# Kernel tuning notes

Measured on AMD Instinct MI355X. Metric: run time of the kernel, lower is better.

## Reference

```python
import jax, jax.numpy as jnp
import numpy as np

INPUT_DIM = 1024
CODEBOOK_DIM = 128
CODEBOOK_SIZE = 8192
B, N = 8, 4096


def setup_inputs() -> dict:
    key = jax.random.key(0)
    k1, k2, k3 = jax.random.split(key, 3)
    x = jax.random.normal(k1, (B, N, INPUT_DIM), dtype=jnp.float32)
    # xavier_normal_: std = sqrt(2 / (fan_in + fan_out))
    xavier_std = float(np.sqrt(2.0 / (INPUT_DIM + CODEBOOK_DIM)))
    random_projection = jax.random.normal(k2, (INPUT_DIM, CODEBOOK_DIM), dtype=jnp.float32) * xavier_std
    codebook = jax.random.normal(k3, (CODEBOOK_SIZE, CODEBOOK_DIM), dtype=jnp.float32)
    return {"x": x, "random_projection": random_projection, "codebook": codebook}


def reference(x, random_projection, codebook):
    # random projection: [B, N, D] @ [D, E] -> [B, N, E]
    proj = jnp.einsum("bnd,de->bne", x, random_projection)
    b, n, e = proj.shape
    flat = proj.reshape(b * n, e)  # [BN, E]
    eps = 1e-12  # matches torch F.normalize default eps
    nx = flat / jnp.maximum(jnp.linalg.norm(flat, axis=1, keepdims=True), eps)
    ncb = codebook / jnp.maximum(jnp.linalg.norm(codebook, axis=1, keepdims=True), eps)
    # squared euclidean distances [K, BN]; argmin of d^2 == argmin of cdist
    d2 = (
        jnp.sum(ncb * ncb, axis=1)[:, None]
        + jnp.sum(nx * nx, axis=1)[None, :]
        - 2.0 * (ncb @ nx.T)
    )
    nearest = jnp.argmin(d2, axis=0)  # [BN]
    return nearest.reshape(b, n).astype(jnp.int32)
```

## Files before the change

kernel.cpp:

```cpp
#include <hip/hip_runtime.h>
#include <math.h>
#include <float.h>
#include <limits.h>

#define BN      32768
#define D_IN    1024
#define E_DIM   128
#define CB_N    8192

typedef _Float16 f16x8 __attribute__((ext_vector_type(8)));
typedef _Float16 f16x4 __attribute__((ext_vector_type(4)));
typedef float    f32x4 __attribute__((ext_vector_type(4)));


__global__ __launch_bounds__(256) void pack_cb_kernel(
    const float* __restrict__ cb, _Float16* __restrict__ ph,
    _Float16* __restrict__ pl) {
    __shared__ float L[16][129];
    const int t = threadIdx.x;
    const int g = blockIdx.x;

    const int c = t >> 4, p = t & 15;
    const float4 v0 = *(const float4*)&cb[(size_t)(g * 16 + c) * E_DIM + p * 8];
    const float4 v1 = *(const float4*)&cb[(size_t)(g * 16 + c) * E_DIM + p * 8 + 4];
    float ss = v0.x * v0.x + v0.y * v0.y + v0.z * v0.z + v0.w * v0.w
             + v1.x * v1.x + v1.y * v1.y + v1.z * v1.z + v1.w * v1.w;
#pragma unroll
    for (int m = 1; m < 16; m <<= 1) ss += __shfl_xor(ss, m);
    const float inv = 256.0f / fmaxf(sqrtf(ss), 1e-12f);

    L[c][p * 8 + 0] = v0.x * inv; L[c][p * 8 + 1] = v0.y * inv;
    L[c][p * 8 + 2] = v0.z * inv; L[c][p * 8 + 3] = v0.w * inv;
    L[c][p * 8 + 4] = v1.x * inv; L[c][p * 8 + 5] = v1.y * inv;
    L[c][p * 8 + 6] = v1.z * inv; L[c][p * 8 + 7] = v1.w * inv;
    __syncthreads();

    const int kb = t >> 6, lane = t & 63;
    const int quad = (lane >> 4), col = lane & 15;
    f16x8 h, l;
#pragma unroll
    for (int j = 0; j < 8; ++j) {
        const float v = L[col][kb * 32 + quad * 8 + j];
        const _Float16 hv = (_Float16)v;
        h[j] = hv;
        l[j] = (_Float16)(v - (float)hv);
    }
    const size_t off = ((size_t)(g * 4 + kb) * 64 + lane) * 8;
    *(f16x8*)&ph[off] = h;
    *(f16x8*)&pl[off] = l;
}

__global__ __launch_bounds__(64) void pack_rp_kernel(
    const float* __restrict__ rp, _Float16* __restrict__ rph,
    _Float16* __restrict__ rpl) {
    const int b = blockIdx.x;
    const int kb = b >> 3, nt = b & 7;
    const int lane = threadIdx.x;
    const int quad = lane >> 4, col = lane & 15;
    f16x8 h, l;
#pragma unroll
    for (int j = 0; j < 8; ++j) {
        const float v = rp[(size_t)(kb * 32 + quad * 8 + j) * E_DIM + nt * 16 + col] * 64.0f;
        const _Float16 hv = (_Float16)v;
        h[j] = hv;
        l[j] = (_Float16)(v - (float)hv);
    }
    const size_t off = ((size_t)b * 64 + lane) * 8;
    *(f16x8*)&rph[off] = h;
    *(f16x8*)&rpl[off] = l;
}

#define PAD_ROW 40
#define PPITCH  132

__global__ __launch_bounds__(256, 2) void fused_kernel(
    const float* __restrict__ x,
    const _Float16* __restrict__ rph, const _Float16* __restrict__ rpl,
    const _Float16* __restrict__ ph, const _Float16* __restrict__ pl,
    int* __restrict__ out) {
    __shared__ _Float16 Ah[64 * PAD_ROW];
    __shared__ _Float16 Al[64 * PAD_ROW];
    __shared__ float    P[64 * PPITCH];
    __shared__ float    ls[4][32];
    __shared__ int      li[4][32];

    const int tid  = threadIdx.x;
    const int lane = tid & 63;
    const int w    = tid >> 6;
    const int quad = lane >> 4, col = lane & 15;
    const int qb   = blockIdx.x * 64;

    const int srow = tid >> 3;
    const int skc  = (tid & 7) * 4;

    f32x4 acc[4][2];
#pragma unroll
    for (int mt = 0; mt < 4; ++mt)
#pragma unroll
        for (int h = 0; h < 2; ++h) acc[mt][h] = (f32x4){0.f, 0.f, 0.f, 0.f};

    float4 pre[2];
#pragma unroll
    for (int i = 0; i < 2; ++i)
        pre[i] = *(const float4*)&x[(size_t)(qb + srow + 32 * i) * D_IN + skc];

    for (int kb = 0; kb < 32; ++kb) {
#pragma unroll
        for (int i = 0; i < 2; ++i) {
            const float vv[4] = {pre[i].x, pre[i].y, pre[i].z, pre[i].w};
            f16x4 h4, l4;
#pragma unroll
            for (int j = 0; j < 4; ++j) {
                const float v = vv[j] * 512.0f;
                const _Float16 hv = (_Float16)v;
                h4[j] = hv;
                l4[j] = (_Float16)(v - (float)hv);
            }
            const int base = (srow + 32 * i) * PAD_ROW + skc;
            *(f16x4*)&Ah[base] = h4;
            *(f16x4*)&Al[base] = l4;
        }
        __syncthreads();

        if (kb + 1 < 32) {
#pragma unroll
            for (int i = 0; i < 2; ++i)
                pre[i] = *(const float4*)&x[(size_t)(qb + srow + 32 * i) * D_IN + (kb + 1) * 32 + skc];
        }

        f16x8 bh1[2], bl1[2];
#pragma unroll
        for (int h = 0; h < 2; ++h) {
            const int nt = w * 2 + h;
            const size_t off = ((size_t)(kb * 8 + nt) * 64 + lane) * 8;
            bh1[h] = *(const f16x8*)&rph[off];
            bl1[h] = *(const f16x8*)&rpl[off];
        }

        f16x8 ah1[4], al1[4];
#pragma unroll
        for (int mt = 0; mt < 4; ++mt) {
            const int base = (mt * 16 + col) * PAD_ROW + quad * 8;
            ah1[mt] = *(const f16x8*)&Ah[base];
            al1[mt] = *(const f16x8*)&Al[base];
        }

#pragma unroll
        for (int mt = 0; mt < 4; ++mt)
#pragma unroll
            for (int h = 0; h < 2; ++h)
                acc[mt][h] = __builtin_amdgcn_mfma_f32_16x16x32_f16(ah1[mt], bh1[h], acc[mt][h], 0, 0, 0);
#pragma unroll
        for (int mt = 0; mt < 4; ++mt)
#pragma unroll
            for (int h = 0; h < 2; ++h)
                acc[mt][h] = __builtin_amdgcn_mfma_f32_16x16x32_f16(ah1[mt], bl1[h], acc[mt][h], 0, 0, 0);
#pragma unroll
        for (int mt = 0; mt < 4; ++mt)
#pragma unroll
            for (int h = 0; h < 2; ++h)
                acc[mt][h] = __builtin_amdgcn_mfma_f32_16x16x32_f16(al1[mt], bh1[h], acc[mt][h], 0, 0, 0);

        __syncthreads();
    }

#pragma unroll
    for (int mt = 0; mt < 4; ++mt)
#pragma unroll
        for (int h = 0; h < 2; ++h)
#pragma unroll
            for (int r = 0; r < 4; ++r) {
                const int row = mt * 16 + quad * 4 + r;
                const int cc  = w * 32 + h * 16 + col;
                P[row * PPITCH + cc] = acc[mt][h][r] * (1.0f / 2048.0f);
            }
    __syncthreads();

    const int wq = w >> 1;
    const int wc = w & 1;

    f16x8 ah[2][4], al[2][4];
#pragma unroll
    for (int mt2 = 0; mt2 < 2; ++mt2)
#pragma unroll
        for (int kb = 0; kb < 4; ++kb) {
            const int base = (wq * 32 + mt2 * 16 + col) * PPITCH + kb * 32 + quad * 8;
            const float4 v0 = *(const float4*)&P[base];
            const float4 v1 = *(const float4*)&P[base + 4];
            const float vv[8] = {v0.x, v0.y, v0.z, v0.w, v1.x, v1.y, v1.z, v1.w};
            f16x8 hh, ll;
#pragma unroll
            for (int j = 0; j < 8; ++j) {
                const _Float16 hv = (_Float16)vv[j];
                hh[j] = hv;
                ll[j] = (_Float16)(vv[j] - (float)hv);
            }
            ah[mt2][kb] = hh;
            al[mt2][kb] = ll;
        }

    float bs[8];
    int   bi[8];
#pragma unroll
    for (int s = 0; s < 8; ++s) { bs[s] = -FLT_MAX; bi[s] = 0; }

    const int g0 = wc * 256;

    f16x8 bh[2][4], bl[2][4];
#pragma unroll
    for (int kb = 0; kb < 4; ++kb) {
        const size_t off = ((size_t)(g0 * 4 + kb) * 64 + lane) * 8;
        bh[0][kb] = *(const f16x8*)&ph[off];
        bl[0][kb] = *(const f16x8*)&pl[off];
    }

#pragma unroll 2
    for (int t = 0; t < 256; ++t) {
        const int cur = t & 1, nxt = cur ^ 1;
        if (t + 1 < 256) {
            const int gn = g0 + t + 1;
#pragma unroll
            for (int kb = 0; kb < 4; ++kb) {
                const size_t off = ((size_t)(gn * 4 + kb) * 64 + lane) * 8;
                bh[nxt][kb] = *(const f16x8*)&ph[off];
                bl[nxt][kb] = *(const f16x8*)&pl[off];
            }
        }

        f32x4 sacc[2];
#pragma unroll
        for (int mt2 = 0; mt2 < 2; ++mt2) sacc[mt2] = (f32x4){0.f, 0.f, 0.f, 0.f};

#pragma unroll
        for (int kb = 0; kb < 4; ++kb)
#pragma unroll
            for (int mt2 = 0; mt2 < 2; ++mt2)
                sacc[mt2] = __builtin_amdgcn_mfma_f32_16x16x32_f16(ah[mt2][kb], bh[cur][kb], sacc[mt2], 0, 0, 0);
#pragma unroll
        for (int kb = 0; kb < 4; ++kb)
#pragma unroll
            for (int mt2 = 0; mt2 < 2; ++mt2)
                sacc[mt2] = __builtin_amdgcn_mfma_f32_16x16x32_f16(ah[mt2][kb], bl[cur][kb], sacc[mt2], 0, 0, 0);
#pragma unroll
        for (int kb = 0; kb < 4; ++kb)
#pragma unroll
            for (int mt2 = 0; mt2 < 2; ++mt2)
                sacc[mt2] = __builtin_amdgcn_mfma_f32_16x16x32_f16(al[mt2][kb], bh[cur][kb], sacc[mt2], 0, 0, 0);

        const int code = (g0 + t) * 16 + col;
#pragma unroll
        for (int mt2 = 0; mt2 < 2; ++mt2)
#pragma unroll
            for (int r = 0; r < 4; ++r) {
                const float v = sacc[mt2][r];
                const int s = mt2 * 4 + r;
                if (v > bs[s]) { bs[s] = v; bi[s] = code; }
            }
    }

#pragma unroll
    for (int s = 0; s < 8; ++s) {
#pragma unroll
        for (int m = 1; m < 16; m <<= 1) {
            const float os = __shfl_xor(bs[s], m);
            const int   oi = __shfl_xor(bi[s], m);
            if (os > bs[s] || (os == bs[s] && oi < bi[s])) { bs[s] = os; bi[s] = oi; }
        }
    }

    if (col == 0) {
#pragma unroll
        for (int mt2 = 0; mt2 < 2; ++mt2)
#pragma unroll
            for (int r = 0; r < 4; ++r) {
                ls[w][mt2 * 16 + quad * 4 + r] = bs[mt2 * 4 + r];
                li[w][mt2 * 16 + quad * 4 + r] = bi[mt2 * 4 + r];
            }
    }
    __syncthreads();

    if (tid < 64) {
        const int q   = tid;
        const int wq2 = q >> 5;
        const int q32 = q & 31;
        float s = ls[wq2 * 2 + 0][q32];
        int   i = li[wq2 * 2 + 0][q32];
        const float os = ls[wq2 * 2 + 1][q32];
        if (os > s) { s = os; i = li[wq2 * 2 + 1][q32]; }
        out[qb + q] = i;
    }
}

extern "C" void kernel_launch(void* const* d_in, const int* in_sizes, int n_in,
                              void* d_out, int out_size, void* d_ws, size_t ws_size,
                              hipStream_t stream) {
    const float* x  = (const float*)d_in[0];
    const float* rp = (const float*)d_in[1];
    const float* cb = (const float*)d_in[2];
    int* out = (int*)d_out;

    _Float16* ph  = (_Float16*)d_ws;
    _Float16* pl  = ph  + (size_t)CB_N * E_DIM;
    _Float16* rph = pl  + (size_t)CB_N * E_DIM;
    _Float16* rpl = rph + (size_t)D_IN * E_DIM;

    pack_cb_kernel<<<CB_N / 16, 256, 0, stream>>>(cb, ph, pl);
    pack_rp_kernel<<<256, 64, 0, stream>>>(rp, rph, rpl);
    fused_kernel<<<BN / 64, 256, 0, stream>>>(x, rph, rpl, ph, pl, out);
}
```

Baseline: 409.7 us.

## Load x directly into MFMA registers, drop LDS staging, merge pack kernels

The projection GEMM stage now has each lane load its own fp32 x fragments straight from global memory into MFMA operand layout and split them into fp16 hi/lo in registers. This removes the shared-memory staging buffers and the two block barriers per k-step. The random-projection fragments are now prefetched one step ahead. The two pack kernels are merged into one launch, with the rp path staged through LDS for coalesced reads, and s_setprio is raised around the distance MFMA block. The cost is less coalesced x loads (32-byte segments per row) and higher register pressure.

```diff
diff --git a/kernel.cpp b/kernel.cpp
--- a/kernel.cpp
+++ b/kernel.cpp
@@ -13,64 +13,75 @@
 typedef float    f32x4 __attribute__((ext_vector_type(4)));
 
 
-__global__ __launch_bounds__(256) void pack_cb_kernel(
+__global__ __launch_bounds__(256) void pack_all_kernel(
     const float* __restrict__ cb, _Float16* __restrict__ ph,
-    _Float16* __restrict__ pl) {
-    __shared__ float L[16][129];
-    const int t = threadIdx.x;
-    const int g = blockIdx.x;
-
-    const int c = t >> 4, p = t & 15;
-    const float4 v0 = *(const float4*)&cb[(size_t)(g * 16 + c) * E_DIM + p * 8];
-    const float4 v1 = *(const float4*)&cb[(size_t)(g * 16 + c) * E_DIM + p * 8 + 4];
-    float ss = v0.x * v0.x + v0.y * v0.y + v0.z * v0.z + v0.w * v0.w
-             + v1.x * v1.x + v1.y * v1.y + v1.z * v1.z + v1.w * v1.w;
-#pragma unroll
-    for (int m = 1; m < 16; m <<= 1) ss += __shfl_xor(ss, m);
-    const float inv = 256.0f / fmaxf(sqrtf(ss), 1e-12f);
-
-    L[c][p * 8 + 0] = v0.x * inv; L[c][p * 8 + 1] = v0.y * inv;
-    L[c][p * 8 + 2] = v0.z * inv; L[c][p * 8 + 3] = v0.w * inv;
-    L[c][p * 8 + 4] = v1.x * inv; L[c][p * 8 + 5] = v1.y * inv;
-    L[c][p * 8 + 6] = v1.z * inv; L[c][p * 8 + 7] = v1.w * inv;
-    __syncthreads();
-
-    const int kb = t >> 6, lane = t & 63;
-    const int quad = (lane >> 4), col = lane & 15;
-    f16x8 h, l;
-#pragma unroll
-    for (int j = 0; j < 8; ++j) {
-        const float v = L[col][kb * 32 + quad * 8 + j];
-        const _Float16 hv = (_Float16)v;
-        h[j] = hv;
-        l[j] = (_Float16)(v - (float)hv);
-    }
-    const size_t off = ((size_t)(g * 4 + kb) * 64 + lane) * 8;
-    *(f16x8*)&ph[off] = h;
-    *(f16x8*)&pl[off] = l;
-}
-
-__global__ __launch_bounds__(64) void pack_rp_kernel(
+    _Float16* __restrict__ pl,
     const float* __restrict__ rp, _Float16* __restrict__ rph,
     _Float16* __restrict__ rpl) {
+    __shared__ float L[16][129];
+    __shared__ float R[32][132];
+    const int t = threadIdx.x;
     const int b = blockIdx.x;
-    const int kb = b >> 3, nt = b & 7;
-    const int lane = threadIdx.x;
-    const int quad = lane >> 4, col = lane & 15;
-    f16x8 h, l;
-#pragma unroll
-    for (int j = 0; j < 8; ++j) {
-        const float v = rp[(size_t)(kb * 32 + quad * 8 + j) * E_DIM + nt * 16 + col] * 64.0f;
-        const _Float16 hv = (_Float16)v;
-        h[j] = hv;
-        l[j] = (_Float16)(v - (float)hv);
-    }
-    const size_t off = ((size_t)b * 64 + lane) * 8;
-    *(f16x8*)&rph[off] = h;
-    *(f16x8*)&rpl[off] = l;
+
+    if (b < 512) {
+        const int g = b;
+        const int c = t >> 4, p = t & 15;
+        const float4 v0 = *(const float4*)&cb[(size_t)(g * 16 + c) * E_DIM + p * 8];
+        const float4 v1 = *(const float4*)&cb[(size_t)(g * 16 + c) * E_DIM + p * 8 + 4];
+        float ss = v0.x * v0.x + v0.y * v0.y + v0.z * v0.z + v0.w * v0.w
+                 + v1.x * v1.x + v1.y * v1.y + v1.z * v1.z + v1.w * v1.w;
+#pragma unroll
+        for (int m = 1; m < 16; m <<= 1) ss += __shfl_xor(ss, m);
+        const float inv = 256.0f / fmaxf(sqrtf(ss), 1e-12f);
+
+        L[c][p * 8 + 0] = v0.x * inv; L[c][p * 8 + 1] = v0.y * inv;
+        L[c][p * 8 + 2] = v0.z * inv; L[c][p * 8 + 3] = v0.w * inv;
+        L[c][p * 8 + 4] = v1.x * inv; L[c][p * 8 + 5] = v1.y * inv;
+        L[c][p * 8 + 6] = v1.z * inv; L[c][p * 8 + 7] = v1.w * inv;
+        __syncthreads();
+
+        const int kb = t >> 6, lane = t & 63;
+        const int quad = (lane >> 4), col = lane & 15;
+        f16x8 h, l;
+#pragma unroll
+        for (int j = 0; j < 8; ++j) {
+            const float v = L[col][kb * 32 + quad * 8 + j];
+            const _Float16 hv = (_Float16)v;
+            h[j] = hv;
+            l[j] = (_Float16)(v - (float)hv);
+        }
+        const size_t off = ((size_t)(g * 4 + kb) * 64 + lane) * 8;
+        *(f16x8*)&ph[off] = h;
+        *(f16x8*)&pl[off] = l;
+    } else {
+        const int kb = b - 512;
+        const int r = t >> 3, c0 = (t & 7) * 16;
+#pragma unroll
+        for (int i = 0; i < 4; ++i)
+            *(float4*)&R[r][c0 + i * 4] =
+                *(const float4*)&rp[(size_t)(kb * 32 + r) * E_DIM + c0 + i * 4];
+        __syncthreads();
+
+        const int w = t >> 6, lane = t & 63;
+        const int quad = lane >> 4, col = lane & 15;
+#pragma unroll
+        for (int h2 = 0; h2 < 2; ++h2) {
+            const int nt = w * 2 + h2;
+            f16x8 hh, ll;
+#pragma unroll
+            for (int j = 0; j < 8; ++j) {
+                const float v = R[quad * 8 + j][nt * 16 + col] * 64.0f;
+                const _Float16 hv = (_Float16)v;
+                hh[j] = hv;
+                ll[j] = (_Float16)(v - (float)hv);
+            }
+            const size_t off = ((size_t)((kb * 8 + nt) * 64) + lane) * 8;
+            *(f16x8*)&rph[off] = hh;
+            *(f16x8*)&rpl[off] = ll;
+        }
+    }
 }
 
-#define PAD_ROW 40
 #define PPITCH  132
 
 __global__ __launch_bounds__(256, 2) void fused_kernel(
@@ -78,8 +89,6 @@
     const _Float16* __restrict__ rph, const _Float16* __restrict__ rpl,
     const _Float16* __restrict__ ph, const _Float16* __restrict__ pl,
     int* __restrict__ out) {
-    __shared__ _Float16 Ah[64 * PAD_ROW];
-    __shared__ _Float16 Al[64 * PAD_ROW];
     __shared__ float    P[64 * PPITCH];
     __shared__ float    ls[4][32];
     __shared__ int      li[4][32];
@@ -90,8 +99,10 @@
     const int quad = lane >> 4, col = lane & 15;
     const int qb   = blockIdx.x * 64;
 
-    const int srow = tid >> 3;
-    const int skc  = (tid & 7) * 4;
+    const float* xr[4];
+#pragma unroll
+    for (int mt = 0; mt < 4; ++mt)
+        xr[mt] = x + (size_t)(qb + mt * 16 + col) * D_IN + quad * 8;
 
     f32x4 acc[4][2];
 #pragma unroll
@@ -99,50 +110,55 @@
 #pragma unroll
         for (int h = 0; h < 2; ++h) acc[mt][h] = (f32x4){0.f, 0.f, 0.f, 0.f};
 
-    float4 pre[2];
-#pragma unroll
-    for (int i = 0; i < 2; ++i)
-        pre[i] = *(const float4*)&x[(size_t)(qb + srow + 32 * i) * D_IN + skc];
+    float4 pA[4][2];
+#pragma unroll
+    for (int mt = 0; mt < 4; ++mt) {
+        pA[mt][0] = *(const float4*)(xr[mt] + 0);
+        pA[mt][1] = *(const float4*)(xr[mt] + 4);
+    }
+    f16x8 bhc[2], blc[2];
+#pragma unroll
+    for (int h = 0; h < 2; ++h) {
+        const size_t off = ((size_t)(w * 2 + h) * 64 + lane) * 8;
+        bhc[h] = *(const f16x8*)&rph[off];
+        blc[h] = *(const f16x8*)&rpl[off];
+    }
 
     for (int kb = 0; kb < 32; ++kb) {
-#pragma unroll
-        for (int i = 0; i < 2; ++i) {
-            const float vv[4] = {pre[i].x, pre[i].y, pre[i].z, pre[i].w};
-            f16x4 h4, l4;
-#pragma unroll
-            for (int j = 0; j < 4; ++j) {
+        f16x8 ah1[4], al1[4];
+#pragma unroll
+        for (int mt = 0; mt < 4; ++mt) {
+            const float vv[8] = {pA[mt][0].x, pA[mt][0].y, pA[mt][0].z, pA[mt][0].w,
+                                 pA[mt][1].x, pA[mt][1].y, pA[mt][1].z, pA[mt][1].w};
+            f16x8 hh, ll;
+#pragma unroll
+            for (int j = 0; j < 8; ++j) {
                 const float v = vv[j] * 512.0f;
                 const _Float16 hv = (_Float16)v;
-                h4[j] = hv;
-                l4[j] = (_Float16)(v - (float)hv);
-            }
-            const int base = (srow + 32 * i) * PAD_ROW + skc;
-            *(f16x4*)&Ah[base] = h4;
-            *(f16x4*)&Al[base] = l4;
-        }
-        __syncthreads();
+                hh[j] = hv;
+                ll[j] = (_Float16)(v - (float)hv);
+            }
+            ah1[mt] = hh;
+            al1[mt] = ll;
+        }
 
         if (kb + 1 < 32) {
 #pragma unroll
-            for (int i = 0; i < 2; ++i)
-                pre[i] = *(const float4*)&x[(size_t)(qb + srow + 32 * i) * D_IN + (kb + 1) * 32 + skc];
-        }
-
-        f16x8 bh1[2], bl1[2];
-#pragma unroll
-        for (int h = 0; h < 2; ++h) {
-            const int nt = w * 2 + h;
-            const size_t off = ((size_t)(kb * 8 + nt) * 64 + lane) * 8;
-            bh1[h] = *(const f16x8*)&rph[off];
-            bl1[h] = *(const f16x8*)&rpl[off];
-        }
-
-        f16x8 ah1[4], al1[4];
-#pragma unroll
-        for (int mt = 0; mt < 4; ++mt) {
-            const int base = (mt * 16 + col) * PAD_ROW + quad * 8;
-            ah1[mt] = *(const f16x8*)&Ah[base];
-            al1[mt] = *(const f16x8*)&Al[base];
+            for (int mt = 0; mt < 4; ++mt) {
+                pA[mt][0] = *(const float4*)(xr[mt] + (kb + 1) * 32);
+                pA[mt][1] = *(const float4*)(xr[mt] + (kb + 1) * 32 + 4);
+            }
+        }
+
+        f16x8 bh1[2] = {bhc[0], bhc[1]};
+        f16x8 bl1[2] = {blc[0], blc[1]};
+        if (kb + 1 < 32) {
+#pragma unroll
+            for (int h = 0; h < 2; ++h) {
+                const size_t off = ((size_t)((kb + 1) * 8 + w * 2 + h) * 64 + lane) * 8;
+                bhc[h] = *(const f16x8*)&rph[off];
+                blc[h] = *(const f16x8*)&rpl[off];
+            }
         }
 
 #pragma unroll
@@ -160,8 +176,6 @@
 #pragma unroll
             for (int h = 0; h < 2; ++h)
                 acc[mt][h] = __builtin_amdgcn_mfma_f32_16x16x32_f16(al1[mt], bh1[h], acc[mt][h], 0, 0, 0);
-
-        __syncthreads();
     }
 
 #pragma unroll
@@ -231,6 +245,7 @@
 #pragma unroll
         for (int mt2 = 0; mt2 < 2; ++mt2) sacc[mt2] = (f32x4){0.f, 0.f, 0.f, 0.f};
 
+        __builtin_amdgcn_s_setprio(1);
 #pragma unroll
         for (int kb = 0; kb < 4; ++kb)
 #pragma unroll
@@ -246,6 +261,7 @@
 #pragma unroll
             for (int mt2 = 0; mt2 < 2; ++mt2)
                 sacc[mt2] = __builtin_amdgcn_mfma_f32_16x16x32_f16(al[mt2][kb], bh[cur][kb], sacc[mt2], 0, 0, 0);
+        __builtin_amdgcn_s_setprio(0);
 
         const int code = (g0 + t) * 16 + col;
 #pragma unroll
@@ -304,7 +320,6 @@
     _Float16* rph = pl  + (size_t)CB_N * E_DIM;
     _Float16* rpl = rph + (size_t)D_IN * E_DIM;
 
-    pack_cb_kernel<<<CB_N / 16, 256, 0, stream>>>(cb, ph, pl);
-    pack_rp_kernel<<<256, 64, 0, stream>>>(rp, rph, rpl);
+    pack_all_kernel<<<CB_N / 16 + 32, 256, 0, stream>>>(cb, ph, pl, rp, rph, rpl);
     fused_kernel<<<BN / 64, 256, 0, stream>>>(x, rph, rpl, ph, pl, out);
 }
```

Measured after the change: 392.6 us. 4.2% less time.
